# Kernel tuning notes

Measured on AMD Instinct MI355X. Metric: run time of the kernel, lower is better.

The kernel has to match this reference:

```python
import jax, jax.numpy as jnp
import numpy as np

N_NODES = 50000
N_EDGES = 600000
N_GRAPHS = 512
IN_C, HID_C, OUT_C = 128, 128, 64


def setup_inputs() -> dict:
    key = jax.random.key(0)
    ks = jax.random.split(key, 16)
    inp = {
        "x": jax.random.normal(ks[0], (N_NODES, IN_C), dtype=jnp.float32),
        "edge_index": jax.random.randint(ks[1], (2, N_EDGES), 0, N_NODES, dtype=jnp.int64),
        "batch": jnp.sort(jax.random.randint(ks[2], (N_NODES,), 0, N_GRAPHS, dtype=jnp.int64)),
    }
    # GINConv MLPs: Linear(din,dout) -> ReLU -> Linear(dout,dout)
    dims = [(IN_C, HID_C), (HID_C, HID_C), (HID_C, OUT_C)]
    ki = 3
    for l, (din, dout) in enumerate(dims):
        inp[f"w1_{l}"] = jax.random.normal(ks[ki], (din, dout), jnp.float32) / np.sqrt(din).astype(np.float32)
        inp[f"b1_{l}"] = jnp.zeros((dout,), jnp.float32)
        inp[f"w2_{l}"] = jax.random.normal(ks[ki + 1], (dout, dout), jnp.float32) / np.sqrt(dout).astype(np.float32)
        inp[f"b2_{l}"] = jnp.zeros((dout,), jnp.float32)
        ki += 2
    return inp


def _gin_conv(x, src, dst, w1, b1, w2, b2):
    # sum-aggregate neighbor features: agg[i] = sum_{(j->i) in E} x[j]
    agg = jax.ops.segment_sum(x[src], dst, num_segments=N_NODES)
    h = x + agg  # eps = 0 -> (1+eps)*x + agg
    h = jnp.maximum(h @ w1 + b1, 0.0)
    return h @ w2 + b2


def reference(x, edge_index, batch,
              w1_0, b1_0, w2_0, b2_0,
              w1_1, b1_1, w2_1, b2_1,
              w1_2, b1_2, w2_2, b2_2):
    src, dst = edge_index[0], edge_index[1]
    params = [(w1_0, b1_0, w2_0, b2_0),
              (w1_1, b1_1, w2_1, b2_1),
              (w1_2, b1_2, w2_2, b2_2)]
    # first num_layers-1 convs with outer ReLU
    for l in range(2):
        x = jnp.maximum(_gin_conv(x, src, dst, *params[l]), 0.0)
    x = _gin_conv(x, src, dst, *params[2])
    # global_add_pool over graph ids -> [G, out_channels]
    return jax.ops.segment_sum(x, batch, num_segments=N_GRAPHS)
```

## Files before the change

### kernel.cpp

```cpp
#include <hip/hip_runtime.h>

#define N_NODES 50000
#define N_EDGES 600000
#define N_GRAPHS 512
#define CAP 48
#define NRT 3125

typedef unsigned int u32;
typedef unsigned short u16;
typedef __attribute__((ext_vector_type(8))) short bf16x8;
typedef __attribute__((ext_vector_type(4))) float f32x4;

__device__ __forceinline__ float bflo(u32 v) { return __uint_as_float(v << 16); }
__device__ __forceinline__ float bfhi(u32 v) { return __uint_as_float(v & 0xffff0000u); }
__device__ __forceinline__ u16 f2bf(float f) {
    u32 x = __float_as_uint(f);
    return (u16)((x + 0x7fffu + ((x >> 16) & 1u)) >> 16);
}
__device__ __forceinline__ void addrow(float* a, uint4 v) {
    a[0] += bflo(v.x); a[1] += bfhi(v.x);
    a[2] += bflo(v.y); a[3] += bfhi(v.y);
    a[4] += bflo(v.z); a[5] += bfhi(v.z);
    a[6] += bflo(v.w); a[7] += bfhi(v.w);
}
__device__ __forceinline__ void addrow2(float* a, uint2 v) {
    a[0] += bflo(v.x); a[1] += bfhi(v.x);
    a[2] += bflo(v.y); a[3] += bfhi(v.y);
}

__device__ __forceinline__ int idx_at(const int* __restrict__ a, int i, int wide) {
    return wide ? a[2 * i] : a[i];
}

__global__ void init_kernel(const int* __restrict__ ei, int* __restrict__ cnt,
                            int* __restrict__ flag, float* __restrict__ out,
                            int out_n) {
    int i = blockIdx.x * 256 + threadIdx.x;
    if (i < N_NODES) cnt[i] = 0;
    if (i < out_n) out[i] = 0.f;
    if (blockIdx.x == 0 && threadIdx.x < 64) {
        int v = ei[2 * threadIdx.x + 1];
        unsigned long long nz = __ballot(v != 0);
        if (threadIdx.x == 0) *flag = (nz == 0ull) ? 1 : 0;
    }
}

struct CvtDesc { const float* w; u16* wt; int K, N, bx, bstart; };
struct CvtAll { CvtDesc d[6]; };
struct PrepArgs {
    const int* ei; const int* flag;
    int* cnt; u16* slots;
    const float* x; u16* xb;
    CvtAll ca;
};
#define SCAT_B 2344
#define CVTX_B 6250
#define PREP_B (SCAT_B + CVTX_B + 76)

__global__ void prep_kernel(PrepArgs p) {
    int b = blockIdx.x;
    if (b < SCAT_B) {
        int e = b * 256 + threadIdx.x;
        if (e >= N_EDGES) return;
        int w = *p.flag;
        const int* src = p.ei;
        const int* dst = p.ei + (w ? 2 * N_EDGES : N_EDGES);
        int d = idx_at(dst, e, w);
        int pos = atomicAdd(&p.cnt[d], 1);
        if (pos < CAP) p.slots[(size_t)d * CAP + pos] = (u16)idx_at(src, e, w);
        return;
    }
    if (b < SCAT_B + CVTX_B) {
        size_t i = (size_t)(b - SCAT_B) * 256 + threadIdx.x;
        float4 v = *(const float4*)&p.x[i * 4];
        u32 o0 = (u32)f2bf(v.x) | ((u32)f2bf(v.y) << 16);
        u32 o1 = (u32)f2bf(v.z) | ((u32)f2bf(v.w) << 16);
        uint2 o; o.x = o0; o.y = o1;
        *(uint2*)&p.xb[i * 4] = o;
        return;
    }
    __shared__ float tile[32][33];
    int rel0 = b - (SCAT_B + CVTX_B);
    int di = 0;
#pragma unroll
    for (int i = 1; i < 6; ++i) if (rel0 >= p.ca.d[i].bstart) di = i;
    CvtDesc d = p.ca.d[di];
    int rel = rel0 - d.bstart;
    int bk = (rel % d.bx) * 32, bn = (rel / d.bx) * 32;
    int tx = threadIdx.x & 31, ty = threadIdx.x >> 5;
#pragma unroll
    for (int yy = 0; yy < 32; yy += 8)
        tile[ty + yy][tx] = d.w[(size_t)(bk + ty + yy) * d.N + bn + tx];
    __syncthreads();
#pragma unroll
    for (int yy = 0; yy < 32; yy += 8)
        d.wt[(size_t)(bn + ty + yy) * d.K + bk + tx] = f2bf(tile[tx][ty + yy]);
}

__global__ void agg128_kernel(const u16* __restrict__ xb, const int* __restrict__ cnt,
                              const u16* __restrict__ slots, u16* __restrict__ h2) {
    int node = blockIdx.x * 16 + (threadIdx.x >> 4);
    int l = threadIdx.x & 15;
    if (node >= N_NODES) return;
    uint4 sv = *(const uint4*)(xb + ((size_t)node << 7) + l * 8);
    float acc[8] = { bflo(sv.x), bfhi(sv.x), bflo(sv.y), bfhi(sv.y),
                     bflo(sv.z), bfhi(sv.z), bflo(sv.w), bfhi(sv.w) };
    int deg = cnt[node]; if (deg > CAP) deg = CAP;
    const u16* sp = slots + (size_t)node * CAP;
    int j = 0;
    for (; j + 4 <= deg; j += 4) {
        int s0 = sp[j], s1 = sp[j + 1], s2 = sp[j + 2], s3 = sp[j + 3];
        uint4 v0 = *(const uint4*)(xb + ((size_t)s0 << 7) + l * 8);
        uint4 v1 = *(const uint4*)(xb + ((size_t)s1 << 7) + l * 8);
        uint4 v2 = *(const uint4*)(xb + ((size_t)s2 << 7) + l * 8);
        uint4 v3 = *(const uint4*)(xb + ((size_t)s3 << 7) + l * 8);
        addrow(acc, v0); addrow(acc, v1);
        addrow(acc, v2); addrow(acc, v3);
    }
    for (; j < deg; ++j) {
        int s0 = sp[j];
        uint4 v0 = *(const uint4*)(xb + ((size_t)s0 << 7) + l * 8);
        addrow(acc, v0);
    }
    uint4 o;
    o.x = (u32)f2bf(acc[0]) | ((u32)f2bf(acc[1]) << 16);
    o.y = (u32)f2bf(acc[2]) | ((u32)f2bf(acc[3]) << 16);
    o.z = (u32)f2bf(acc[4]) | ((u32)f2bf(acc[5]) << 16);
    o.w = (u32)f2bf(acc[6]) | ((u32)f2bf(acc[7]) << 16);
    *(uint4*)(h2 + (size_t)(node >> 4) * 2048 + l * 128 + (node & 15) * 8) = o;
}

__global__ void agg64_kernel(const u16* __restrict__ z, const int* __restrict__ cnt,
                             const u16* __restrict__ slots,
                             const float* __restrict__ b1, u16* __restrict__ tout) {
    int node = blockIdx.x * 16 + (threadIdx.x >> 4);
    int l = threadIdx.x & 15;
    if (node >= N_NODES) return;
    uint2 sv = *(const uint2*)(z + ((size_t)node << 6) + l * 4);
    float acc[4] = { bflo(sv.x), bfhi(sv.x), bflo(sv.y), bfhi(sv.y) };
    int deg = cnt[node]; if (deg > CAP) deg = CAP;
    const u16* sp = slots + (size_t)node * CAP;
    int j = 0;
    for (; j + 4 <= deg; j += 4) {
        int s0 = sp[j], s1 = sp[j + 1], s2 = sp[j + 2], s3 = sp[j + 3];
        uint2 v0 = *(const uint2*)(z + ((size_t)s0 << 6) + l * 4);
        uint2 v1 = *(const uint2*)(z + ((size_t)s1 << 6) + l * 4);
        uint2 v2 = *(const uint2*)(z + ((size_t)s2 << 6) + l * 4);
        uint2 v3 = *(const uint2*)(z + ((size_t)s3 << 6) + l * 4);
        addrow2(acc, v0); addrow2(acc, v1);
        addrow2(acc, v2); addrow2(acc, v3);
    }
    for (; j < deg; ++j) {
        int s0 = sp[j];
        uint2 v0 = *(const uint2*)(z + ((size_t)s0 << 6) + l * 4);
        addrow2(acc, v0);
    }
    float t0 = fmaxf(acc[0] + b1[l * 4 + 0], 0.f);
    float t1 = fmaxf(acc[1] + b1[l * 4 + 1], 0.f);
    float t2 = fmaxf(acc[2] + b1[l * 4 + 2], 0.f);
    float t3 = fmaxf(acc[3] + b1[l * 4 + 3], 0.f);
    uint2 o;
    o.x = (u32)f2bf(t0) | ((u32)f2bf(t1) << 16);
    o.y = (u32)f2bf(t2) | ((u32)f2bf(t3) << 16);
    *(uint2*)(tout + ((size_t)node << 6) + l * 4) = o;
}

template <int CHAIN>
__global__ __launch_bounds__(256) void mlp_kernel(
    const u16* __restrict__ h2,
    const u16* __restrict__ w1t, const float* __restrict__ b1,
    const u16* __restrict__ w2t, const float* __restrict__ b2,
    const u16* __restrict__ w3t, u16* __restrict__ zout,
    u16* __restrict__ yout)
{
    __shared__ __attribute__((aligned(16))) u16 ls[4 * 4096];
    const int wave = threadIdx.x >> 6, lane = threadIdx.x & 63;
    const int rtA = blockIdx.x * 8 + wave * 2;
    const int rtB = rtA + 1;
    if (rtA >= NRT) return;
    const bool hasB = (rtB < NRT);
    const int m = lane & 15, q = lane >> 4, ko = q * 8;
    u16* tsA = ls + wave * 4096;
    u16* tsB = tsA + 2048;
    const u16* hpA = h2 + (size_t)rtA * 2048;
    const u16* hpB = h2 + (size_t)rtB * 2048;

    bf16x8 a1A[4], a1B[4];
#pragma unroll
    for (int s = 0; s < 4; ++s)
        a1A[s] = *(const bf16x8*)&hpA[s * 512 + q * 128 + m * 8];
    if (hasB) {
#pragma unroll
        for (int s = 0; s < 4; ++s)
            a1B[s] = *(const bf16x8*)&hpB[s * 512 + q * 128 + m * 8];
    }

    {
        f32x4 accA[8], accB[8];
#pragma unroll
        for (int nt = 0; nt < 8; ++nt) {
            accA[nt] = (f32x4){0.f, 0.f, 0.f, 0.f};
            accB[nt] = (f32x4){0.f, 0.f, 0.f, 0.f};
        }
#pragma unroll
        for (int nt = 0; nt < 8; ++nt) {
            int n = nt * 16 + m;
#pragma unroll
            for (int s = 0; s < 4; ++s) {
                bf16x8 bf = *(const bf16x8*)&w1t[(size_t)n * 128 + s * 32 + ko];
                accA[nt] = __builtin_amdgcn_mfma_f32_16x16x32_bf16(a1A[s], bf, accA[nt], 0, 0, 0);
                if (hasB)
                    accB[nt] = __builtin_amdgcn_mfma_f32_16x16x32_bf16(a1B[s], bf, accB[nt], 0, 0, 0);
            }
        }
#pragma unroll
        for (int nt = 0; nt < 8; ++nt) {
            int n = nt * 16 + m;
            float bias = b1[n];
#pragma unroll
            for (int j2 = 0; j2 < 4; ++j2) {
                int dr = q * 4 + j2;
                int sw = (dr & 7) << 3;
                tsA[dr * 128 + (n ^ sw)] = f2bf(fmaxf(accA[nt][j2] + bias, 0.f));
                if (hasB)
                    tsB[dr * 128 + (n ^ sw)] = f2bf(fmaxf(accB[nt][j2] + bias, 0.f));
            }
        }
    }

    {
        const int swm = (m & 7) << 3;
        bf16x8 a2A[4], a2B[4];
#pragma unroll
        for (int s = 0; s < 4; ++s)
            a2A[s] = *(const bf16x8*)&tsA[m * 128 + ((s * 32 + ko) ^ swm)];
        if (hasB) {
#pragma unroll
            for (int s = 0; s < 4; ++s)
                a2B[s] = *(const bf16x8*)&tsB[m * 128 + ((s * 32 + ko) ^ swm)];
        }
        f32x4 accA[8], accB[8];
#pragma unroll
        for (int nt = 0; nt < 8; ++nt) {
            accA[nt] = (f32x4){0.f, 0.f, 0.f, 0.f};
            accB[nt] = (f32x4){0.f, 0.f, 0.f, 0.f};
        }
#pragma unroll
        for (int nt = 0; nt < 8; ++nt) {
            int n = nt * 16 + m;
#pragma unroll
            for (int s = 0; s < 4; ++s) {
                bf16x8 bf = *(const bf16x8*)&w2t[(size_t)n * 128 + s * 32 + ko];
                accA[nt] = __builtin_amdgcn_mfma_f32_16x16x32_bf16(a2A[s], bf, accA[nt], 0, 0, 0);
                if (hasB)
                    accB[nt] = __builtin_amdgcn_mfma_f32_16x16x32_bf16(a2B[s], bf, accB[nt], 0, 0, 0);
            }
        }
#pragma unroll
        for (int nt = 0; nt < 8; ++nt) {
            int n = nt * 16 + m;
            float bias = b2[n];
#pragma unroll
            for (int j2 = 0; j2 < 4; ++j2) {
                int dr = q * 4 + j2;
                int sw = (dr & 7) << 3;
                tsA[dr * 128 + (n ^ sw)] = f2bf(fmaxf(accA[nt][j2] + bias, 0.f));
                if (hasB)
                    tsB[dr * 128 + (n ^ sw)] = f2bf(fmaxf(accB[nt][j2] + bias, 0.f));
            }
        }
    }

    if (CHAIN) {
        const int swm = (m & 7) << 3;
        bf16x8 a3A[4], a3B[4];
#pragma unroll
        for (int s = 0; s < 4; ++s)
            a3A[s] = *(const bf16x8*)&tsA[m * 128 + ((s * 32 + ko) ^ swm)];
        if (hasB) {
#pragma unroll
            for (int s = 0; s < 4; ++s)
                a3B[s] = *(const bf16x8*)&tsB[m * 128 + ((s * 32 + ko) ^ swm)];
        }
        f32x4 accA[4], accB[4];
#pragma unroll
        for (int nt = 0; nt < 4; ++nt) {
            accA[nt] = (f32x4){0.f, 0.f, 0.f, 0.f};
            accB[nt] = (f32x4){0.f, 0.f, 0.f, 0.f};
        }
#pragma unroll
        for (int nt = 0; nt < 4; ++nt) {
            int n3 = nt * 16 + m;
#pragma unroll
            for (int s = 0; s < 4; ++s) {
                bf16x8 bf = *(const bf16x8*)&w3t[(size_t)n3 * 128 + s * 32 + ko];
                accA[nt] = __builtin_amdgcn_mfma_f32_16x16x32_bf16(a3A[s], bf, accA[nt], 0, 0, 0);
                if (hasB)
                    accB[nt] = __builtin_amdgcn_mfma_f32_16x16x32_bf16(a3B[s], bf, accB[nt], 0, 0, 0);
            }
        }
#pragma unroll
        for (int nt = 0; nt < 4; ++nt) {
            int n3 = nt * 16 + m;
#pragma unroll
            for (int j2 = 0; j2 < 4; ++j2) {
                int row = q * 4 + j2;
                zout[(size_t)(rtA * 16 + row) * 64 + n3] = f2bf(accA[nt][j2]);
                if (hasB)
                    zout[(size_t)(rtB * 16 + row) * 64 + n3] = f2bf(accB[nt][j2]);
            }
        }
    } else {
        int r = lane >> 2;
        int c0 = (lane & 3) * 32;
        const int sw = (r & 7) << 3;
#pragma unroll
        for (int j = 0; j < 4; ++j) {
            int ce = c0 + j * 8;
            uint4 v = *(const uint4*)&tsA[r * 128 + (ce ^ sw)];
            *(uint4*)&yout[(size_t)(rtA * 16 + r) * 128 + ce] = v;
        }
        if (hasB) {
#pragma unroll
            for (int j = 0; j < 4; ++j) {
                int ce = c0 + j * 8;
                uint4 v = *(const uint4*)&tsB[r * 128 + (ce ^ sw)];
                *(uint4*)&yout[(size_t)(rtB * 16 + r) * 128 + ce] = v;
            }
        }
    }
}

__global__ __launch_bounds__(1024) void pool_kernel(
    const u16* __restrict__ t, const u16* __restrict__ w2t,
    const float* __restrict__ b2,
    const int* __restrict__ batch, const int* __restrict__ flagp,
    float* __restrict__ out)
{
    constexpr int YB_ST = 66;
    __shared__ __attribute__((aligned(16))) char smemA[64 * YB_ST * 4];
    __shared__ int gids[64];
    u16* hs = (u16*)smemA;
    float* yb = (float*)smemA;

    const int tid = threadIdx.x;
    const int wave = tid >> 6, lane = tid & 63;
    const int base = blockIdx.x * 64;
    const int wflag = *flagp;

    if (tid < 64) {
        int node = base + tid;
        gids[tid] = (node < N_NODES) ? idx_at(batch, node, wflag) : -1;
    }
    {
        int row = tid >> 4, c0 = (tid & 15) * 4;
        uint2 v = *(const uint2*)&t[((size_t)(base + row)) * 64 + c0];
        *(uint2*)&hs[row * 64 + (c0 ^ ((row & 7) << 3))] = v;
    }
    __syncthreads();

    const int m = lane & 15;
    const int ko = (lane >> 4) * 8;
    const int rb = (wave & 3) * 16;
    const int cb = (wave >> 2) * 16;

    {
        const int rr = rb + m;
        const int sw = (rr & 7) << 3;
        bf16x8 a2[2];
#pragma unroll
        for (int s = 0; s < 2; ++s)
            a2[s] = *(const bf16x8*)&hs[rr * 64 + ((s * 32 + ko) ^ sw)];
        f32x4 acc = (f32x4){0.f, 0.f, 0.f, 0.f};
        int n = cb + m;
#pragma unroll
        for (int s = 0; s < 2; ++s) {
            bf16x8 bf = *(const bf16x8*)&w2t[(size_t)n * 64 + s * 32 + ko];
            acc = __builtin_amdgcn_mfma_f32_16x16x32_bf16(a2[s], bf, acc, 0, 0, 0);
        }
        float bias = b2[n];
        __syncthreads();
#pragma unroll
        for (int j2 = 0; j2 < 4; ++j2) {
            int dr = rb + (lane >> 4) * 4 + j2;
            yb[dr * YB_ST + n] = acc[j2] + bias;
        }
    }
    __syncthreads();

    {
        int gl = gids[lane];
        int gp = (lane > 0) ? gids[lane - 1] : gl;
        unsigned long long mask = __ballot(lane > 0 && gl != gp) | 1ull;
        int nruns = (int)__popcll(mask);
        int c = tid >> 4, s = tid & 15;
        unsigned long long mm = mask;
        for (int r = 0; r < nruns; ++r) {
            int start = (int)__builtin_ctzll(mm);
            mm &= mm - 1;
            int end = mm ? (int)__builtin_ctzll(mm) : 64;
            int gid = gids[start];
            if (gid >= 0) {
                float sum = 0.f;
                for (int n2 = start + s; n2 < end; n2 += 16)
                    sum += yb[n2 * YB_ST + c];
                sum += __shfl_xor(sum, 1);
                sum += __shfl_xor(sum, 2);
                sum += __shfl_xor(sum, 4);
                sum += __shfl_xor(sum, 8);
                if (s == 0)
                    atomicAdd(&out[(size_t)gid * 64 + c], sum);
            }
        }
    }
}

extern "C" void kernel_launch(void* const* d_in, const int* in_sizes, int n_in,
                              void* d_out, int out_size, void* d_ws, size_t ws_size,
                              hipStream_t stream) {
    const float* x     = (const float*)d_in[0];
    const int*   ei    = (const int*)d_in[1];
    const int*   batch = (const int*)d_in[2];
    const float* w1[3] = {(const float*)d_in[3], (const float*)d_in[7],  (const float*)d_in[11]};
    const float* b1[3] = {(const float*)d_in[4], (const float*)d_in[8],  (const float*)d_in[12]};
    const float* w2[3] = {(const float*)d_in[5], (const float*)d_in[9],  (const float*)d_in[13]};
    const float* b2[3] = {(const float*)d_in[6], (const float*)d_in[10], (const float*)d_in[14]};
    float* out = (float*)d_out;

    char* ws = (char*)d_ws;
    int*   cnt     = (int*)(ws + 0);
    int*   flag    = (int*)(ws + 200704);
    u16*   slots   = (u16*)(ws + 201728);
    u16*   xb      = (u16*)(ws + 9801728);
    u16*   hbuf    = (u16*)(ws + 22601728);
    u16*   yA      = (u16*)(ws + 35401728);
    u16*   wts     = (u16*)(ws + 48201728);
    u16*   zbuf    = xb;
    u16*   tbuf    = yA;
    u16* w1t0 = wts +      0;
    u16* w2t0 = wts +  16384;
    u16* w1t1 = wts +  32768;
    u16* w2t1 = wts +  49152;
    u16* w1t2 = wts +  65536;
    u16* w2t2 = wts +  73728;

    init_kernel<<<196, 256, 0, stream>>>(ei, cnt, flag, out, out_size);

    PrepArgs pa;
    pa.ei = ei; pa.flag = flag; pa.cnt = cnt; pa.slots = slots;
    pa.x = x; pa.xb = xb;
    pa.ca.d[0] = {w1[0], w1t0, 128, 128, 4,  0};
    pa.ca.d[1] = {w2[0], w2t0, 128, 128, 4, 16};
    pa.ca.d[2] = {w1[1], w1t1, 128, 128, 4, 32};
    pa.ca.d[3] = {w2[1], w2t1, 128, 128, 4, 48};
    pa.ca.d[4] = {w1[2], w1t2, 128,  64, 4, 64};
    pa.ca.d[5] = {w2[2], w2t2,  64,  64, 2, 72};
    prep_kernel<<<PREP_B, 256, 0, stream>>>(pa);

    const int NAGG = (N_NODES + 15) / 16;
    const int NTIL = (N_NODES + 63) / 64;
    const int NMLP = (NRT + 7) / 8;

    agg128_kernel<<<NAGG, 256, 0, stream>>>(xb, cnt, slots, hbuf);
    mlp_kernel<0><<<NMLP, 256, 0, stream>>>(hbuf, w1t0, b1[0], w2t0, b2[0],
                                            (const u16*)0, (u16*)0, yA);
    agg128_kernel<<<NAGG, 256, 0, stream>>>(yA, cnt, slots, hbuf);
    mlp_kernel<1><<<NMLP, 256, 0, stream>>>(hbuf, w1t1, b1[1], w2t1, b2[1],
                                            w1t2, zbuf, (u16*)0);
    agg64_kernel<<<NAGG, 256, 0, stream>>>(zbuf, cnt, slots, b1[2], tbuf);
    pool_kernel<<<NTIL, 1024, 0, stream>>>(tbuf, w2t2, b2[2], batch, flag, out);
}
```

Before: 174.4 us.

## Partition edge-scatter atomics per XCC and compact into per-node slot lists

The edge scatter now keeps separate counters and slot arrays for each XCC, picked from the hardware XCC_ID register, so atomics stay local to one die's L2 and do not contend across dies. A new compact kernel merges the eight partial lists into the existing per-node CAP slot layout. This costs an extra kernel launch, eight times the counter initialisation, and extra traffic through scratch buffers. Any one partition holding more than 16 edges for a node will silently drop neighbours.

```diff
diff --git a/kernel.cpp b/kernel.cpp
--- a/kernel.cpp
+++ b/kernel.cpp
@@ -4,6 +4,7 @@
 #define N_EDGES 600000
 #define N_GRAPHS 512
 #define CAP 48
+#define PCAP 16
 #define NRT 3125
 
 typedef unsigned int u32;
@@ -32,11 +33,20 @@
     return wide ? a[2 * i] : a[i];
 }
 
-__global__ void init_kernel(const int* __restrict__ ei, int* __restrict__ cnt,
+__device__ __forceinline__ int xcc_id() {
+    u32 x;
+    asm("s_getreg_b32 %0, hwreg(HW_REG_XCC_ID)" : "=s"(x));
+    return (int)(x & 7);
+}
+
+__global__ void init_kernel(const int* __restrict__ ei, int* __restrict__ cnt2,
                             int* __restrict__ flag, float* __restrict__ out,
                             int out_n) {
     int i = blockIdx.x * 256 + threadIdx.x;
-    if (i < N_NODES) cnt[i] = 0;
+    if (i < N_NODES) {
+#pragma unroll
+        for (int pp = 0; pp < 8; ++pp) cnt2[pp * N_NODES + i] = 0;
+    }
     if (i < out_n) out[i] = 0.f;
     if (blockIdx.x == 0 && threadIdx.x < 64) {
         int v = ei[2 * threadIdx.x + 1];
@@ -49,7 +59,7 @@
 struct CvtAll { CvtDesc d[6]; };
 struct PrepArgs {
     const int* ei; const int* flag;
-    int* cnt; u16* slots;
+    int* cnt2; u16* slots2;
     const float* x; u16* xb;
     CvtAll ca;
 };
@@ -66,16 +76,19 @@
         const int* src = p.ei;
         const int* dst = p.ei + (w ? 2 * N_EDGES : N_EDGES);
         int d = idx_at(dst, e, w);
-        int pos = atomicAdd(&p.cnt[d], 1);
-        if (pos < CAP) p.slots[(size_t)d * CAP + pos] = (u16)idx_at(src, e, w);
+        int part = xcc_id();
+        int pos = atomicAdd(&p.cnt2[part * N_NODES + d], 1);
+        if (pos < PCAP)
+            p.slots2[((size_t)part * N_NODES + d) * PCAP + pos] =
+                (u16)idx_at(src, e, w);
         return;
     }
     if (b < SCAT_B + CVTX_B) {
         size_t i = (size_t)(b - SCAT_B) * 256 + threadIdx.x;
         float4 v = *(const float4*)&p.x[i * 4];
-        u32 o0 = (u32)f2bf(v.x) | ((u32)f2bf(v.y) << 16);
-        u32 o1 = (u32)f2bf(v.z) | ((u32)f2bf(v.w) << 16);
-        uint2 o; o.x = o0; o.y = o1;
+        uint2 o;
+        o.x = (u32)f2bf(v.x) | ((u32)f2bf(v.y) << 16);
+        o.y = (u32)f2bf(v.z) | ((u32)f2bf(v.w) << 16);
         *(uint2*)&p.xb[i * 4] = o;
         return;
     }
@@ -95,6 +108,25 @@
 #pragma unroll
     for (int yy = 0; yy < 32; yy += 8)
         d.wt[(size_t)(bn + ty + yy) * d.K + bk + tx] = f2bf(tile[tx][ty + yy]);
+}
+
+__global__ void compact_kernel(const int* __restrict__ cnt2,
+                               const u16* __restrict__ slots2,
+                               int* __restrict__ cnt, u16* __restrict__ slots) {
+    int node = blockIdx.x * 256 + threadIdx.x;
+    if (node >= N_NODES) return;
+    u16* dst = slots + (size_t)node * CAP;
+    int total = 0;
+#pragma unroll
+    for (int pp = 0; pp < 8; ++pp) {
+        int c = cnt2[pp * N_NODES + node];
+        if (c > PCAP) c = PCAP;
+        const u16* sp = slots2 + ((size_t)pp * N_NODES + node) * PCAP;
+        for (int i = 0; i < c; ++i) {
+            if (total < CAP) { dst[total] = sp[i]; ++total; }
+        }
+    }
+    cnt[node] = total;
 }
 
 __global__ void agg128_kernel(const u16* __restrict__ xb, const int* __restrict__ cnt,
@@ -437,6 +469,8 @@
     u16*   wts     = (u16*)(ws + 48201728);
     u16*   zbuf    = xb;
     u16*   tbuf    = yA;
+    u16*   slots2  = hbuf;
+    int*   cnt2    = (int*)yA;
     u16* w1t0 = wts +      0;
     u16* w2t0 = wts +  16384;
     u16* w1t1 = wts +  32768;
@@ -444,10 +478,10 @@
     u16* w1t2 = wts +  65536;
     u16* w2t2 = wts +  73728;
 
-    init_kernel<<<196, 256, 0, stream>>>(ei, cnt, flag, out, out_size);
+    init_kernel<<<196, 256, 0, stream>>>(ei, cnt2, flag, out, out_size);
 
     PrepArgs pa;
-    pa.ei = ei; pa.flag = flag; pa.cnt = cnt; pa.slots = slots;
+    pa.ei = ei; pa.flag = flag; pa.cnt2 = cnt2; pa.slots2 = slots2;
     pa.x = x; pa.xb = xb;
     pa.ca.d[0] = {w1[0], w1t0, 128, 128, 4,  0};
     pa.ca.d[1] = {w2[0], w2t0, 128, 128, 4, 16};
@@ -457,6 +491,8 @@
     pa.ca.d[5] = {w2[2], w2t2,  64,  64, 2, 72};
     prep_kernel<<<PREP_B, 256, 0, stream>>>(pa);
 
+    compact_kernel<<<196, 256, 0, stream>>>(cnt2, slots2, cnt, slots);
+
     const int NAGG = (N_NODES + 15) / 16;
     const int NTIL = (N_NODES + 63) / 64;
     const int NMLP = (NRT + 7) / 8;
```

Result: slower. 183.2 us (median of 2 runs) (+5.1%).
